# Kernel tuning notes

Measured on AMD Instinct MI355X. Metric: run time of the kernel, lower is better.

Reference implementation:

```python
import jax, jax.numpy as jnp
import numpy as np

B, T, D_IN = 64, 4096, 3
C1, H, NCLS = 64, 128, 40
BN_EPS = 1e-5


def setup_inputs() -> dict:
    key = jax.random.key(0)
    ks = jax.random.split(key, 12)
    s_ih = 1.0 / np.sqrt(C1)
    s_hh = 1.0 / np.sqrt(H)
    return {
        "x": jax.random.normal(ks[0], (B, T, D_IN), jnp.float32),
        "conv_w": jax.random.normal(ks[1], (C1, D_IN), jnp.float32) * 0.3,
        "conv_b": jax.random.normal(ks[2], (C1,), jnp.float32) * 0.1,
        "bn_gamma": jnp.ones((C1,), jnp.float32),
        "bn_beta": jnp.zeros((C1,), jnp.float32),
        "w_ih": jax.random.normal(ks[3], (4 * H, C1), jnp.float32) * s_ih,
        "b_ih": jax.random.normal(ks[4], (4 * H,), jnp.float32) * s_ih,
        "w_hh": jax.random.normal(ks[5], (4 * H, H), jnp.float32) * s_hh,
        "b_hh": jax.random.normal(ks[6], (4 * H,), jnp.float32) * s_hh,
        "out_w": jax.random.normal(ks[7], (NCLS, H), jnp.float32) * s_hh,
        "out_b": jax.random.normal(ks[8], (NCLS,), jnp.float32) * s_hh,
        "h0": jax.random.normal(ks[9], (B, H), jnp.float32),
        "c0": jax.random.normal(ks[10], (B, H), jnp.float32),
    }


def reference(x, conv_w, conv_b, bn_gamma, bn_beta, w_ih, b_ih, w_hh, b_hh,
              out_w, out_b, h0, c0):
    # Conv1d with kernel_size=1 == pointwise linear over channel dim.
    y = jnp.einsum('btc,oc->bto', x, conv_w) + conv_b  # [B, T, 64]
    # BatchNorm1d in training mode: batch stats over (batch, length).
    mean = jnp.mean(y, axis=(0, 1))
    var = jnp.var(y, axis=(0, 1))  # biased, matches torch BN normalization
    y = (y - mean) * jax.lax.rsqrt(var + BN_EPS) * bn_gamma + bn_beta
    y = jax.nn.relu(y)

    def step(carry, xt):
        h, c = carry
        gates = xt @ w_ih.T + b_ih + h @ w_hh.T + b_hh  # [B, 4H]
        i, f, g, o = jnp.split(gates, 4, axis=-1)
        c = jax.nn.sigmoid(f) * c + jax.nn.sigmoid(i) * jnp.tanh(g)
        h = jax.nn.sigmoid(o) * jnp.tanh(c)
        return (h, c), None

    (hT, _), _ = jax.lax.scan(step, (h0, c0), jnp.swapaxes(y, 0, 1))
    # Only the last hidden state feeds the classifier (output[:, -1, :]).
    return hT @ out_w.T + out_b  # [B, 40]
```

## Files before the change

kernel.cpp:

```cpp
#include <hip/hip_runtime.h>
#include <cstdint>
#include <cstddef>

#define B_    64
#define T_    4096
#define H_    128
#define C1_   64
#define NCLS_ 40

#define LOG2E_     1.4426950408889634f
#define TWOLOG2E_  2.8853900817779268f
#define NEG4LOG2E_ (-5.7707801635558536f)

typedef _Float16 half2_t __attribute__((ext_vector_type(2)));
typedef _Float16 half8_t __attribute__((ext_vector_type(8)));
typedef float    f32x4_t __attribute__((ext_vector_type(4)));

__device__ __forceinline__ half2_t pack2(float a, float b){
  half2_t r; r.x = (_Float16)a; r.y = (_Float16)b; return r;
}

__global__ __launch_bounds__(256) void stats_kernel(const float* __restrict__ x,
                                                    float* __restrict__ stats){
  int t = blockIdx.x * 256 + threadIdx.x;
  const float4* xv = (const float4*)x + (size_t)t * 3;
  float4 a = xv[0], b = xv[1], c = xv[2];
  float x0[4] = {a.x, a.w, b.z, c.y};
  float x1[4] = {a.y, b.x, b.w, c.z};
  float x2[4] = {a.z, b.y, c.x, c.w};
  float s[9] = {0,0,0,0,0,0,0,0,0};
  #pragma unroll
  for (int r=0;r<4;++r){
    s[0]+=x0[r]; s[1]+=x1[r]; s[2]+=x2[r];
    s[3]+=x0[r]*x0[r]; s[4]+=x0[r]*x1[r]; s[5]+=x0[r]*x2[r];
    s[6]+=x1[r]*x1[r]; s[7]+=x1[r]*x2[r]; s[8]+=x2[r]*x2[r];
  }
  __shared__ float red[9][256];
  #pragma unroll
  for (int j=0;j<9;++j) red[j][threadIdx.x] = s[j];
  __syncthreads();
  if (threadIdx.x < 9){
    float sum = 0.f;
    for (int i=0;i<256;++i) sum += red[threadIdx.x][i];
    atomicAdd(&stats[threadIdx.x], sum);
  }
}

__device__ __forceinline__ void chan_affine(int c, const float* __restrict__ conv_w,
    const float* __restrict__ bn_g, const float* __restrict__ bn_b,
    const float* __restrict__ stats,
    float& A0, float& A1, float& A2, float& Bc){
  const float Ninv = 1.0f / (float)(B_*T_);
  float m0=stats[0]*Ninv, m1=stats[1]*Ninv, m2=stats[2]*Ninv;
  float c00=stats[3]*Ninv-m0*m0, c01=stats[4]*Ninv-m0*m1, c02=stats[5]*Ninv-m0*m2;
  float c11=stats[6]*Ninv-m1*m1, c12=stats[7]*Ninv-m1*m2, c22=stats[8]*Ninv-m2*m2;
  float w0=conv_w[c*3+0], w1=conv_w[c*3+1], w2=conv_w[c*3+2];
  float var = w0*(w0*c00 + 2.f*(w1*c01 + w2*c02)) + w1*(w1*c11 + 2.f*w2*c12) + w2*w2*c22;
  float sc = bn_g[c] * rsqrtf(var + 1e-5f);
  A0 = w0*sc; A1 = w1*sc; A2 = w2*sc;
  Bc = bn_b[c] - (w0*m0 + w1*m1 + w2*m2)*sc;
}

__global__ __launch_bounds__(512,2) void lstm_fused_kernel(
    const float* __restrict__ x,
    const float* __restrict__ conv_w, const float* __restrict__ bn_g,
    const float* __restrict__ bn_b, const float* __restrict__ stats,
    const float* __restrict__ w_ih, const float* __restrict__ b_ih,
    const float* __restrict__ b_hh, const float* __restrict__ w_hh,
    const float* __restrict__ h0, const float* __restrict__ c0,
    const float* __restrict__ out_w, const float* __restrict__ out_b,
    float* __restrict__ out){
  constexpr int CH   = 16;
  constexpr int PSTR = 516;
  int b = blockIdx.x, t = threadIdx.x;
  int lane = t & 63, wv = t >> 6;
  int rfrag = lane & 15, kgrp = lane >> 4;
  int estar = wv*16 + rfrag;
  bool wrt = (kgrp == 0);

  __shared__ __align__(16) _Float16 hbuf[2][H_];
  __shared__ __align__(16) float P_lds[CH * PSTR];
  __shared__ __align__(16) float4 cf_lds[C1_];

  if (t < C1_){
    float A0,A1,A2,Bc; chan_affine(t, conv_w, bn_g, bn_b, stats, A0,A1,A2,Bc);
    cf_lds[t] = make_float4(A0,A1,A2,Bc);
  }

  half8_t Wf[4][4];
  #pragma unroll
  for (int g=0; g<4; ++g){
    float sg = (g==2) ? TWOLOG2E_ : -LOG2E_;
    #pragma unroll
    for (int kc=0; kc<4; ++kc){
      const float4* wp = (const float4*)(w_hh + (size_t)(g*H_ + wv*16 + rfrag)*H_ + kc*32 + kgrp*8);
      float4 u0 = wp[0], u1 = wp[1];
      half8_t hv;
      hv[0]=(_Float16)(sg*u0.x); hv[1]=(_Float16)(sg*u0.y);
      hv[2]=(_Float16)(sg*u0.z); hv[3]=(_Float16)(sg*u0.w);
      hv[4]=(_Float16)(sg*u1.x); hv[5]=(_Float16)(sg*u1.y);
      hv[6]=(_Float16)(sg*u1.z); hv[7]=(_Float16)(sg*u1.w);
      Wf[g][kc] = hv;
    }
  }
  half8_t bf[4][2];
  float sgb[4];
  #pragma unroll
  for (int g=0; g<4; ++g){
    int n = g*H_ + wv*16 + rfrag;
    float sg = (g==2) ? TWOLOG2E_ : -LOG2E_;
    sgb[g] = sg * (b_ih[n] + b_hh[n]);
    #pragma unroll
    for (int kh=0; kh<2; ++kh){
      const float4* wp = (const float4*)(w_ih + (size_t)n*C1_ + kh*32 + kgrp*8);
      float4 u0 = wp[0], u1 = wp[1];
      half8_t hv;
      hv[0]=(_Float16)(sg*u0.x); hv[1]=(_Float16)(sg*u0.y);
      hv[2]=(_Float16)(sg*u0.z); hv[3]=(_Float16)(sg*u0.w);
      hv[4]=(_Float16)(sg*u1.x); hv[5]=(_Float16)(sg*u1.y);
      hv[6]=(_Float16)(sg*u1.z); hv[7]=(_Float16)(sg*u1.w);
      bf[g][kh] = hv;
    }
  }

  float cs = TWOLOG2E_ * c0[(size_t)b*H_ + estar];
  if (wrt) hbuf[0][estar] = (_Float16)h0[(size_t)b*H_ + estar];

  const float* xb = x + (size_t)b*T_*3;
  float xp0, xp1, xp2;
  { const float* p = xb + 3*rfrag; xp0 = p[0]; xp1 = p[1]; xp2 = p[2]; }
  const f32x4_t Z = {0.f, 0.f, 0.f, 0.f};
  __syncthreads();

  for (int c = 0; c < T_/CH; ++c){
    half8_t a0, a1;
    #pragma unroll
    for (int j=0;j<8;++j){
      float4 q = cf_lds[kgrp*8+j];
      a0[j] = (_Float16)fmaxf(fmaf(q.x,xp0, fmaf(q.y,xp1, fmaf(q.z,xp2, q.w))), 0.f);
      float4 rr = cf_lds[32+kgrp*8+j];
      a1[j] = (_Float16)fmaxf(fmaf(rr.x,xp0, fmaf(rr.y,xp1, fmaf(rr.z,xp2, rr.w))), 0.f);
    }
    { int row = (c+1)*CH + rfrag; row = (row < T_) ? row : (T_-1);
      const float* p = xb + 3*row; xp0 = p[0]; xp1 = p[1]; xp2 = p[2]; }
    #pragma unroll
    for (int g=0; g<4; ++g){
      f32x4_t dp = __builtin_amdgcn_mfma_f32_16x16x32_f16(a0, bf[g][0], Z, 0, 0, 0);
      dp = __builtin_amdgcn_mfma_f32_16x16x32_f16(a1, bf[g][1], dp, 0, 0, 0);
      int col = (wv*16 + rfrag)*4 + g;
      #pragma unroll
      for (int v4=0; v4<4; ++v4)
        P_lds[(kgrp*4 + v4)*PSTR + col] = dp[v4] + sgb[g];
    }
    asm volatile("s_waitcnt lgkmcnt(0)" ::: "memory");
    __builtin_amdgcn_s_barrier();
    asm volatile("" ::: "memory");

    f32x4_t pq = *(const f32x4_t*)(P_lds + (size_t)estar*4);

    #pragma unroll
    for (int s=0; s<CH; ++s){
      int p = s & 1;
      if (s > 0){
        asm volatile("s_waitcnt lgkmcnt(0)" ::: "memory");
        __builtin_amdgcn_s_barrier();
        asm volatile("" ::: "memory");
      }
      const _Float16* hb = hbuf[p];
      uint4 hu0 = *(const uint4*)(hb + 0*32 + kgrp*8);
      uint4 hu1 = *(const uint4*)(hb + 1*32 + kgrp*8);
      uint4 hu2 = *(const uint4*)(hb + 2*32 + kgrp*8);
      uint4 hu3 = *(const uint4*)(hb + 3*32 + kgrp*8);
      f32x4_t pqn = pq;
      if (s < CH-1) pqn = *(const f32x4_t*)(P_lds + (size_t)(s+1)*PSTR + estar*4);
      half8_t A0 = __builtin_bit_cast(half8_t, hu0);
      half8_t A1 = __builtin_bit_cast(half8_t, hu1);
      half8_t A2 = __builtin_bit_cast(half8_t, hu2);
      half8_t A3 = __builtin_bit_cast(half8_t, hu3);
      f32x4_t d0 = __builtin_amdgcn_mfma_f32_16x16x32_f16(A0, Wf[0][0], Z, 0,0,0);
      f32x4_t d1 = __builtin_amdgcn_mfma_f32_16x16x32_f16(A0, Wf[1][0], Z, 0,0,0);
      f32x4_t d2 = __builtin_amdgcn_mfma_f32_16x16x32_f16(A0, Wf[2][0], Z, 0,0,0);
      f32x4_t d3 = __builtin_amdgcn_mfma_f32_16x16x32_f16(A0, Wf[3][0], Z, 0,0,0);
      d0 = __builtin_amdgcn_mfma_f32_16x16x32_f16(A1, Wf[0][1], d0, 0,0,0);
      d1 = __builtin_amdgcn_mfma_f32_16x16x32_f16(A1, Wf[1][1], d1, 0,0,0);
      d2 = __builtin_amdgcn_mfma_f32_16x16x32_f16(A1, Wf[2][1], d2, 0,0,0);
      d3 = __builtin_amdgcn_mfma_f32_16x16x32_f16(A1, Wf[3][1], d3, 0,0,0);
      d0 = __builtin_amdgcn_mfma_f32_16x16x32_f16(A2, Wf[0][2], d0, 0,0,0);
      d1 = __builtin_amdgcn_mfma_f32_16x16x32_f16(A2, Wf[1][2], d1, 0,0,0);
      d2 = __builtin_amdgcn_mfma_f32_16x16x32_f16(A2, Wf[2][2], d2, 0,0,0);
      d3 = __builtin_amdgcn_mfma_f32_16x16x32_f16(A2, Wf[3][2], d3, 0,0,0);
      d0 = __builtin_amdgcn_mfma_f32_16x16x32_f16(A3, Wf[0][3], d0, 0,0,0);
      d1 = __builtin_amdgcn_mfma_f32_16x16x32_f16(A3, Wf[1][3], d1, 0,0,0);
      d2 = __builtin_amdgcn_mfma_f32_16x16x32_f16(A3, Wf[2][3], d2, 0,0,0);
      d3 = __builtin_amdgcn_mfma_f32_16x16x32_f16(A3, Wf[3][3], d3, 0,0,0);
      float vI = d0[0] + pq[0];
      float vF = d1[0] + pq[1];
      float vG = d2[0] + pq[2];
      float vO = d3[0] + pq[3];
      float rI = __builtin_amdgcn_rcpf(1.f + __builtin_amdgcn_exp2f(vI));
      float rF = __builtin_amdgcn_rcpf(1.f + __builtin_amdgcn_exp2f(vF));
      float rG = __builtin_amdgcn_rcpf(1.f + __builtin_amdgcn_exp2f(vG));
      float rO = __builtin_amdgcn_rcpf(1.f + __builtin_amdgcn_exp2f(vO));
      float gT2 = fmaf(NEG4LOG2E_, rG, TWOLOG2E_);
      float cn  = fmaf(rF, cs, rI * gT2);
      cs = cn;
      float th = fmaf(-2.f, __builtin_amdgcn_rcpf(1.f + __builtin_amdgcn_exp2f(cn)), 1.f);
      float h  = rO * th;
      if (wrt) hbuf[1-p][estar] = (_Float16)h;
      pq = pqn;
    }
  }
  __syncthreads();
  if (t < NCLS_){
    float s = out_b[t];
    #pragma unroll 8
    for (int kk=0; kk<H_; ++kk)
      s = fmaf(out_w[t*H_ + kk], (float)hbuf[0][kk], s);
    out[(size_t)b*NCLS_ + t] = s;
  }
}

extern "C" void kernel_launch(void* const* d_in, const int* in_sizes, int n_in,
                              void* d_out, int out_size, void* d_ws, size_t ws_size,
                              hipStream_t stream){
  const float* x      = (const float*)d_in[0];
  const float* conv_w = (const float*)d_in[1];
  const float* bn_g   = (const float*)d_in[3];
  const float* bn_b   = (const float*)d_in[4];
  const float* w_ih   = (const float*)d_in[5];
  const float* b_ih   = (const float*)d_in[6];
  const float* w_hh   = (const float*)d_in[7];
  const float* b_hh   = (const float*)d_in[8];
  const float* out_w  = (const float*)d_in[9];
  const float* out_b  = (const float*)d_in[10];
  const float* h0     = (const float*)d_in[11];
  const float* c0     = (const float*)d_in[12];
  float* out   = (float*)d_out;
  float* stats = (float*)d_ws;

  hipMemsetAsync(d_ws, 0, 64, stream);
  stats_kernel<<<256, 256, 0, stream>>>(x, stats);
  lstm_fused_kernel<<<B_, 512, 0, stream>>>(x, conv_w, bn_g, bn_b, stats,
                                            w_ih, b_ih, b_hh, w_hh, h0, c0,
                                            out_w, out_b, out);
}
```

Baseline: 1.684 ms.

## Halve LSTM block to 4 waves, each computing 32 hidden units per step

The fused LSTM kernel now runs 256 threads (4 waves) per batch element instead of 512. Each wave holds recurrent and input weight fragments for two 16-unit tiles and issues 32 MFMAs per timestep. Lanes pick their tile's result with a select, and the P_lds precompute stores become float4 vector writes. The aim is a cheaper per-step barrier across fewer waves, at the cost of doubled MFMA work per wave, roughly double the weight registers, and idle lanes in the gate math.

Measured after the change: 1.856 ms. 1.1x slower.

```diff
diff --git a/kernel.cpp b/kernel.cpp
--- a/kernel.cpp
+++ b/kernel.cpp
@@ -61,7 +61,7 @@
   Bc = bn_b[c] - (w0*m0 + w1*m1 + w2*m2)*sc;
 }
 
-__global__ __launch_bounds__(512,2) void lstm_fused_kernel(
+__global__ __launch_bounds__(256,1) void lstm_fused_kernel(
     const float* __restrict__ x,
     const float* __restrict__ conv_w, const float* __restrict__ bn_g,
     const float* __restrict__ bn_b, const float* __restrict__ stats,
@@ -75,8 +75,10 @@
   int b = blockIdx.x, t = threadIdx.x;
   int lane = t & 63, wv = t >> 6;
   int rfrag = lane & 15, kgrp = lane >> 4;
-  int estar = wv*16 + rfrag;
-  bool wrt = (kgrp == 0);
+  int etl = kgrp >> 1;
+  int estar = wv*32 + etl*16 + rfrag;
+  bool wrt = (kgrp & 1) == 0;
+  bool esel = (etl != 0);
 
   __shared__ __align__(16) _Float16 hbuf[2][H_];
   __shared__ __align__(16) float P_lds[CH * PSTR];
@@ -87,39 +89,45 @@
     cf_lds[t] = make_float4(A0,A1,A2,Bc);
   }
 
-  half8_t Wf[4][4];
+  half8_t Wf[4][2][4];
   #pragma unroll
   for (int g=0; g<4; ++g){
     float sg = (g==2) ? TWOLOG2E_ : -LOG2E_;
     #pragma unroll
-    for (int kc=0; kc<4; ++kc){
-      const float4* wp = (const float4*)(w_hh + (size_t)(g*H_ + wv*16 + rfrag)*H_ + kc*32 + kgrp*8);
-      float4 u0 = wp[0], u1 = wp[1];
-      half8_t hv;
-      hv[0]=(_Float16)(sg*u0.x); hv[1]=(_Float16)(sg*u0.y);
-      hv[2]=(_Float16)(sg*u0.z); hv[3]=(_Float16)(sg*u0.w);
-      hv[4]=(_Float16)(sg*u1.x); hv[5]=(_Float16)(sg*u1.y);
-      hv[6]=(_Float16)(sg*u1.z); hv[7]=(_Float16)(sg*u1.w);
-      Wf[g][kc] = hv;
-    }
-  }
-  half8_t bf[4][2];
-  float sgb[4];
+    for (int et=0; et<2; ++et){
+      #pragma unroll
+      for (int kc=0; kc<4; ++kc){
+        const float4* wp = (const float4*)(w_hh + (size_t)(g*H_ + wv*32 + et*16 + rfrag)*H_ + kc*32 + kgrp*8);
+        float4 u0 = wp[0], u1 = wp[1];
+        half8_t hv;
+        hv[0]=(_Float16)(sg*u0.x); hv[1]=(_Float16)(sg*u0.y);
+        hv[2]=(_Float16)(sg*u0.z); hv[3]=(_Float16)(sg*u0.w);
+        hv[4]=(_Float16)(sg*u1.x); hv[5]=(_Float16)(sg*u1.y);
+        hv[6]=(_Float16)(sg*u1.z); hv[7]=(_Float16)(sg*u1.w);
+        Wf[g][et][kc] = hv;
+      }
+    }
+  }
+  half8_t bf[4][2][2];
+  float sgb[4][2];
   #pragma unroll
   for (int g=0; g<4; ++g){
-    int n = g*H_ + wv*16 + rfrag;
     float sg = (g==2) ? TWOLOG2E_ : -LOG2E_;
-    sgb[g] = sg * (b_ih[n] + b_hh[n]);
-    #pragma unroll
-    for (int kh=0; kh<2; ++kh){
-      const float4* wp = (const float4*)(w_ih + (size_t)n*C1_ + kh*32 + kgrp*8);
-      float4 u0 = wp[0], u1 = wp[1];
-      half8_t hv;
-      hv[0]=(_Float16)(sg*u0.x); hv[1]=(_Float16)(sg*u0.y);
-      hv[2]=(_Float16)(sg*u0.z); hv[3]=(_Float16)(sg*u0.w);
-      hv[4]=(_Float16)(sg*u1.x); hv[5]=(_Float16)(sg*u1.y);
-      hv[6]=(_Float16)(sg*u1.z); hv[7]=(_Float16)(sg*u1.w);
-      bf[g][kh] = hv;
+    #pragma unroll
+    for (int et=0; et<2; ++et){
+      int n = g*H_ + wv*32 + et*16 + rfrag;
+      sgb[g][et] = sg * (b_ih[n] + b_hh[n]);
+      #pragma unroll
+      for (int kh=0; kh<2; ++kh){
+        const float4* wp = (const float4*)(w_ih + (size_t)n*C1_ + kh*32 + kgrp*8);
+        float4 u0 = wp[0], u1 = wp[1];
+        half8_t hv;
+        hv[0]=(_Float16)(sg*u0.x); hv[1]=(_Float16)(sg*u0.y);
+        hv[2]=(_Float16)(sg*u0.z); hv[3]=(_Float16)(sg*u0.w);
+        hv[4]=(_Float16)(sg*u1.x); hv[5]=(_Float16)(sg*u1.y);
+        hv[6]=(_Float16)(sg*u1.z); hv[7]=(_Float16)(sg*u1.w);
+        bf[g][et][kh] = hv;
+      }
     }
   }
 
@@ -143,14 +151,27 @@
     }
     { int row = (c+1)*CH + rfrag; row = (row < T_) ? row : (T_-1);
       const float* p = xb + 3*row; xp0 = p[0]; xp1 = p[1]; xp2 = p[2]; }
+    f32x4_t dp[4][2];
     #pragma unroll
     for (int g=0; g<4; ++g){
-      f32x4_t dp = __builtin_amdgcn_mfma_f32_16x16x32_f16(a0, bf[g][0], Z, 0, 0, 0);
-      dp = __builtin_amdgcn_mfma_f32_16x16x32_f16(a1, bf[g][1], dp, 0, 0, 0);
-      int col = (wv*16 + rfrag)*4 + g;
-      #pragma unroll
-      for (int v4=0; v4<4; ++v4)
-        P_lds[(kgrp*4 + v4)*PSTR + col] = dp[v4] + sgb[g];
+      #pragma unroll
+      for (int et=0; et<2; ++et){
+        f32x4_t d = __builtin_amdgcn_mfma_f32_16x16x32_f16(a0, bf[g][et][0], Z, 0, 0, 0);
+        dp[g][et]  = __builtin_amdgcn_mfma_f32_16x16x32_f16(a1, bf[g][et][1], d, 0, 0, 0);
+      }
+    }
+    #pragma unroll
+    for (int et=0; et<2; ++et){
+      int colbase = (wv*32 + et*16 + rfrag)*4;
+      #pragma unroll
+      for (int v4=0; v4<4; ++v4){
+        f32x4_t vec;
+        vec[0] = dp[0][et][v4] + sgb[0][et];
+        vec[1] = dp[1][et][v4] + sgb[1][et];
+        vec[2] = dp[2][et][v4] + sgb[2][et];
+        vec[3] = dp[3][et][v4] + sgb[3][et];
+        *(f32x4_t*)(P_lds + (size_t)(kgrp*4 + v4)*PSTR + colbase) = vec;
+      }
     }
     asm volatile("s_waitcnt lgkmcnt(0)" ::: "memory");
     __builtin_amdgcn_s_barrier();
@@ -177,26 +198,39 @@
       half8_t A1 = __builtin_bit_cast(half8_t, hu1);
       half8_t A2 = __builtin_bit_cast(half8_t, hu2);
       half8_t A3 = __builtin_bit_cast(half8_t, hu3);
-      f32x4_t d0 = __builtin_amdgcn_mfma_f32_16x16x32_f16(A0, Wf[0][0], Z, 0,0,0);
-      f32x4_t d1 = __builtin_amdgcn_mfma_f32_16x16x32_f16(A0, Wf[1][0], Z, 0,0,0);
-      f32x4_t d2 = __builtin_amdgcn_mfma_f32_16x16x32_f16(A0, Wf[2][0], Z, 0,0,0);
-      f32x4_t d3 = __builtin_amdgcn_mfma_f32_16x16x32_f16(A0, Wf[3][0], Z, 0,0,0);
-      d0 = __builtin_amdgcn_mfma_f32_16x16x32_f16(A1, Wf[0][1], d0, 0,0,0);
-      d1 = __builtin_amdgcn_mfma_f32_16x16x32_f16(A1, Wf[1][1], d1, 0,0,0);
-      d2 = __builtin_amdgcn_mfma_f32_16x16x32_f16(A1, Wf[2][1], d2, 0,0,0);
-      d3 = __builtin_amdgcn_mfma_f32_16x16x32_f16(A1, Wf[3][1], d3, 0,0,0);
-      d0 = __builtin_amdgcn_mfma_f32_16x16x32_f16(A2, Wf[0][2], d0, 0,0,0);
-      d1 = __builtin_amdgcn_mfma_f32_16x16x32_f16(A2, Wf[1][2], d1, 0,0,0);
-      d2 = __builtin_amdgcn_mfma_f32_16x16x32_f16(A2, Wf[2][2], d2, 0,0,0);
-      d3 = __builtin_amdgcn_mfma_f32_16x16x32_f16(A2, Wf[3][2], d3, 0,0,0);
-      d0 = __builtin_amdgcn_mfma_f32_16x16x32_f16(A3, Wf[0][3], d0, 0,0,0);
-      d1 = __builtin_amdgcn_mfma_f32_16x16x32_f16(A3, Wf[1][3], d1, 0,0,0);
-      d2 = __builtin_amdgcn_mfma_f32_16x16x32_f16(A3, Wf[2][3], d2, 0,0,0);
-      d3 = __builtin_amdgcn_mfma_f32_16x16x32_f16(A3, Wf[3][3], d3, 0,0,0);
-      float vI = d0[0] + pq[0];
-      float vF = d1[0] + pq[1];
-      float vG = d2[0] + pq[2];
-      float vO = d3[0] + pq[3];
+      f32x4_t d[4][2];
+      #pragma unroll
+      for (int g=0; g<4; ++g){
+        #pragma unroll
+        for (int et=0; et<2; ++et)
+          d[g][et] = __builtin_amdgcn_mfma_f32_16x16x32_f16(A0, Wf[g][et][0], Z, 0,0,0);
+      }
+      #pragma unroll
+      for (int g=0; g<4; ++g){
+        #pragma unroll
+        for (int et=0; et<2; ++et)
+          d[g][et] = __builtin_amdgcn_mfma_f32_16x16x32_f16(A1, Wf[g][et][1], d[g][et], 0,0,0);
+      }
+      #pragma unroll
+      for (int g=0; g<4; ++g){
+        #pragma unroll
+        for (int et=0; et<2; ++et)
+          d[g][et] = __builtin_amdgcn_mfma_f32_16x16x32_f16(A2, Wf[g][et][2], d[g][et], 0,0,0);
+      }
+      #pragma unroll
+      for (int g=0; g<4; ++g){
+        #pragma unroll
+        for (int et=0; et<2; ++et)
+          d[g][et] = __builtin_amdgcn_mfma_f32_16x16x32_f16(A3, Wf[g][et][3], d[g][et], 0,0,0);
+      }
+      float sI = esel ? d[0][1][0] : d[0][0][0];
+      float sF = esel ? d[1][1][0] : d[1][0][0];
+      float sG = esel ? d[2][1][0] : d[2][0][0];
+      float sO = esel ? d[3][1][0] : d[3][0][0];
+      float vI = sI + pq[0];
+      float vF = sF + pq[1];
+      float vG = sG + pq[2];
+      float vO = sO + pq[3];
       float rI = __builtin_amdgcn_rcpf(1.f + __builtin_amdgcn_exp2f(vI));
       float rF = __builtin_amdgcn_rcpf(1.f + __builtin_amdgcn_exp2f(vF));
       float rG = __builtin_amdgcn_rcpf(1.f + __builtin_amdgcn_exp2f(vG));
@@ -240,7 +274,7 @@
 
   hipMemsetAsync(d_ws, 0, 64, stream);
   stats_kernel<<<256, 256, 0, stream>>>(x, stats);
-  lstm_fused_kernel<<<B_, 512, 0, stream>>>(x, conv_w, bn_g, bn_b, stats,
+  lstm_fused_kernel<<<B_, 256, 0, stream>>>(x, conv_w, bn_g, bn_b, stats,
                                             w_ih, b_ih, b_hh, w_hh, h0, c0,
                                             out_w, out_b, out);
 }
```

## Load hidden state once and broadcast via DPP; split MFMA accumulation chains

Applied to the files above, without the earlier changes.

Each lane now issues a single 16-byte LDS read of the hidden-state slice and uses quad DPP broadcasts to assemble the four A operands, instead of four separate LDS reads per step. The four-deep dependent MFMA accumulation chains are split into two independent chains of two, summed afterwards. Both aim to shorten the per-timestep critical path of the serial recurrence, at the cost of extra DPP VALU instructions and more accumulator registers.

Measured after the change: 2.241 ms. 33.1% more time.

```diff
diff --git a/kernel.cpp b/kernel.cpp
--- a/kernel.cpp
+++ b/kernel.cpp
@@ -18,6 +18,10 @@
 
 __device__ __forceinline__ half2_t pack2(float a, float b){
   half2_t r; r.x = (_Float16)a; r.y = (_Float16)b; return r;
+}
+template<int CTRL>
+__device__ __forceinline__ unsigned qdpp(unsigned x){
+  return (unsigned)__builtin_amdgcn_update_dpp(0, (int)x, CTRL, 0xF, 0xF, true);
 }
 
 __global__ __launch_bounds__(256) void stats_kernel(const float* __restrict__ x,
@@ -130,6 +134,7 @@
   float xp0, xp1, xp2;
   { const float* p = xb + 3*rfrag; xp0 = p[0]; xp1 = p[1]; xp2 = p[2]; }
   const f32x4_t Z = {0.f, 0.f, 0.f, 0.f};
+  int hsl = (lane & 3)*32 + kgrp*8;
   __syncthreads();
 
   for (int c = 0; c < T_/CH; ++c){
@@ -166,37 +171,38 @@
         __builtin_amdgcn_s_barrier();
         asm volatile("" ::: "memory");
       }
-      const _Float16* hb = hbuf[p];
-      uint4 hu0 = *(const uint4*)(hb + 0*32 + kgrp*8);
-      uint4 hu1 = *(const uint4*)(hb + 1*32 + kgrp*8);
-      uint4 hu2 = *(const uint4*)(hb + 2*32 + kgrp*8);
-      uint4 hu3 = *(const uint4*)(hb + 3*32 + kgrp*8);
+      uint4 hr = *(const uint4*)(hbuf[p] + hsl);
       f32x4_t pqn = pq;
       if (s < CH-1) pqn = *(const f32x4_t*)(P_lds + (size_t)(s+1)*PSTR + estar*4);
-      half8_t A0 = __builtin_bit_cast(half8_t, hu0);
-      half8_t A1 = __builtin_bit_cast(half8_t, hu1);
-      half8_t A2 = __builtin_bit_cast(half8_t, hu2);
-      half8_t A3 = __builtin_bit_cast(half8_t, hu3);
-      f32x4_t d0 = __builtin_amdgcn_mfma_f32_16x16x32_f16(A0, Wf[0][0], Z, 0,0,0);
-      f32x4_t d1 = __builtin_amdgcn_mfma_f32_16x16x32_f16(A0, Wf[1][0], Z, 0,0,0);
-      f32x4_t d2 = __builtin_amdgcn_mfma_f32_16x16x32_f16(A0, Wf[2][0], Z, 0,0,0);
-      f32x4_t d3 = __builtin_amdgcn_mfma_f32_16x16x32_f16(A0, Wf[3][0], Z, 0,0,0);
-      d0 = __builtin_amdgcn_mfma_f32_16x16x32_f16(A1, Wf[0][1], d0, 0,0,0);
-      d1 = __builtin_amdgcn_mfma_f32_16x16x32_f16(A1, Wf[1][1], d1, 0,0,0);
-      d2 = __builtin_amdgcn_mfma_f32_16x16x32_f16(A1, Wf[2][1], d2, 0,0,0);
-      d3 = __builtin_amdgcn_mfma_f32_16x16x32_f16(A1, Wf[3][1], d3, 0,0,0);
-      d0 = __builtin_amdgcn_mfma_f32_16x16x32_f16(A2, Wf[0][2], d0, 0,0,0);
-      d1 = __builtin_amdgcn_mfma_f32_16x16x32_f16(A2, Wf[1][2], d1, 0,0,0);
-      d2 = __builtin_amdgcn_mfma_f32_16x16x32_f16(A2, Wf[2][2], d2, 0,0,0);
-      d3 = __builtin_amdgcn_mfma_f32_16x16x32_f16(A2, Wf[3][2], d3, 0,0,0);
-      d0 = __builtin_amdgcn_mfma_f32_16x16x32_f16(A3, Wf[0][3], d0, 0,0,0);
-      d1 = __builtin_amdgcn_mfma_f32_16x16x32_f16(A3, Wf[1][3], d1, 0,0,0);
-      d2 = __builtin_amdgcn_mfma_f32_16x16x32_f16(A3, Wf[2][3], d2, 0,0,0);
-      d3 = __builtin_amdgcn_mfma_f32_16x16x32_f16(A3, Wf[3][3], d3, 0,0,0);
-      float vI = d0[0] + pq[0];
-      float vF = d1[0] + pq[1];
-      float vG = d2[0] + pq[2];
-      float vO = d3[0] + pq[3];
+      uint4 u0, u1, u2, u3;
+      u0.x = qdpp<0x00>(hr.x); u0.y = qdpp<0x00>(hr.y); u0.z = qdpp<0x00>(hr.z); u0.w = qdpp<0x00>(hr.w);
+      u1.x = qdpp<0x55>(hr.x); u1.y = qdpp<0x55>(hr.y); u1.z = qdpp<0x55>(hr.z); u1.w = qdpp<0x55>(hr.w);
+      u2.x = qdpp<0xAA>(hr.x); u2.y = qdpp<0xAA>(hr.y); u2.z = qdpp<0xAA>(hr.z); u2.w = qdpp<0xAA>(hr.w);
+      u3.x = qdpp<0xFF>(hr.x); u3.y = qdpp<0xFF>(hr.y); u3.z = qdpp<0xFF>(hr.z); u3.w = qdpp<0xFF>(hr.w);
+      half8_t A0 = __builtin_bit_cast(half8_t, u0);
+      half8_t A1 = __builtin_bit_cast(half8_t, u1);
+      half8_t A2 = __builtin_bit_cast(half8_t, u2);
+      half8_t A3 = __builtin_bit_cast(half8_t, u3);
+      f32x4_t dA0 = __builtin_amdgcn_mfma_f32_16x16x32_f16(A0, Wf[0][0], Z, 0,0,0);
+      f32x4_t dA1 = __builtin_amdgcn_mfma_f32_16x16x32_f16(A0, Wf[1][0], Z, 0,0,0);
+      f32x4_t dA2 = __builtin_amdgcn_mfma_f32_16x16x32_f16(A0, Wf[2][0], Z, 0,0,0);
+      f32x4_t dA3 = __builtin_amdgcn_mfma_f32_16x16x32_f16(A0, Wf[3][0], Z, 0,0,0);
+      f32x4_t dB0 = __builtin_amdgcn_mfma_f32_16x16x32_f16(A1, Wf[0][1], Z, 0,0,0);
+      f32x4_t dB1 = __builtin_amdgcn_mfma_f32_16x16x32_f16(A1, Wf[1][1], Z, 0,0,0);
+      f32x4_t dB2 = __builtin_amdgcn_mfma_f32_16x16x32_f16(A1, Wf[2][1], Z, 0,0,0);
+      f32x4_t dB3 = __builtin_amdgcn_mfma_f32_16x16x32_f16(A1, Wf[3][1], Z, 0,0,0);
+      dA0 = __builtin_amdgcn_mfma_f32_16x16x32_f16(A2, Wf[0][2], dA0, 0,0,0);
+      dA1 = __builtin_amdgcn_mfma_f32_16x16x32_f16(A2, Wf[1][2], dA1, 0,0,0);
+      dA2 = __builtin_amdgcn_mfma_f32_16x16x32_f16(A2, Wf[2][2], dA2, 0,0,0);
+      dA3 = __builtin_amdgcn_mfma_f32_16x16x32_f16(A2, Wf[3][2], dA3, 0,0,0);
+      dB0 = __builtin_amdgcn_mfma_f32_16x16x32_f16(A3, Wf[0][3], dB0, 0,0,0);
+      dB1 = __builtin_amdgcn_mfma_f32_16x16x32_f16(A3, Wf[1][3], dB1, 0,0,0);
+      dB2 = __builtin_amdgcn_mfma_f32_16x16x32_f16(A3, Wf[2][3], dB2, 0,0,0);
+      dB3 = __builtin_amdgcn_mfma_f32_16x16x32_f16(A3, Wf[3][3], dB3, 0,0,0);
+      float vI = (dA0[0] + dB0[0]) + pq[0];
+      float vF = (dA1[0] + dB1[0]) + pq[1];
+      float vG = (dA2[0] + dB2[0]) + pq[2];
+      float vO = (dA3[0] + dB3[0]) + pq[3];
       float rI = __builtin_amdgcn_rcpf(1.f + __builtin_amdgcn_exp2f(vI));
       float rF = __builtin_amdgcn_rcpf(1.f + __builtin_amdgcn_exp2f(vF));
       float rG = __builtin_amdgcn_rcpf(1.f + __builtin_amdgcn_exp2f(vG));
```

## Process two batch sequences per block to interleave independent LSTM recurrences

Applied to the files above, without the earlier changes.

Each block now handles two batch elements, doubling shared-memory h and preactivation buffers and running both recurrences within the same per-step barrier. The intent is to hide MFMA and transcendental latency of one sequence's serial chain behind the other's and to amortize barrier cost per sequence. It halves the grid and raises register and LDS pressure, and the per-step critical path lengthens if the compiler does not interleave the two chains.

Measured after the change: 3.657 ms. 117% more time.

```diff
diff --git a/kernel.cpp b/kernel.cpp
--- a/kernel.cpp
+++ b/kernel.cpp
@@ -72,14 +72,14 @@
     float* __restrict__ out){
   constexpr int CH   = 16;
   constexpr int PSTR = 516;
-  int b = blockIdx.x, t = threadIdx.x;
+  int bb = blockIdx.x * 2, t = threadIdx.x;
   int lane = t & 63, wv = t >> 6;
   int rfrag = lane & 15, kgrp = lane >> 4;
   int estar = wv*16 + rfrag;
   bool wrt = (kgrp == 0);
 
-  __shared__ __align__(16) _Float16 hbuf[2][H_];
-  __shared__ __align__(16) float P_lds[CH * PSTR];
+  __shared__ __align__(16) _Float16 hbuf[2][2][H_];
+  __shared__ __align__(16) float P_lds[2][CH * PSTR];
   __shared__ __align__(16) float4 cf_lds[C1_];
 
   if (t < C1_){
@@ -123,40 +123,49 @@
     }
   }
 
-  float cs = TWOLOG2E_ * c0[(size_t)b*H_ + estar];
-  if (wrt) hbuf[0][estar] = (_Float16)h0[(size_t)b*H_ + estar];
-
-  const float* xb = x + (size_t)b*T_*3;
-  float xp0, xp1, xp2;
-  { const float* p = xb + 3*rfrag; xp0 = p[0]; xp1 = p[1]; xp2 = p[2]; }
+  float cs[2];
+  float xp[2][3];
+  #pragma unroll
+  for (int ch=0; ch<2; ++ch){
+    cs[ch] = TWOLOG2E_ * c0[(size_t)(bb+ch)*H_ + estar];
+    if (wrt) hbuf[ch][0][estar] = (_Float16)h0[(size_t)(bb+ch)*H_ + estar];
+    const float* p = x + ((size_t)(bb+ch)*T_ + rfrag)*3;
+    xp[ch][0] = p[0]; xp[ch][1] = p[1]; xp[ch][2] = p[2];
+  }
   const f32x4_t Z = {0.f, 0.f, 0.f, 0.f};
   __syncthreads();
 
   for (int c = 0; c < T_/CH; ++c){
-    half8_t a0, a1;
-    #pragma unroll
-    for (int j=0;j<8;++j){
-      float4 q = cf_lds[kgrp*8+j];
-      a0[j] = (_Float16)fmaxf(fmaf(q.x,xp0, fmaf(q.y,xp1, fmaf(q.z,xp2, q.w))), 0.f);
-      float4 rr = cf_lds[32+kgrp*8+j];
-      a1[j] = (_Float16)fmaxf(fmaf(rr.x,xp0, fmaf(rr.y,xp1, fmaf(rr.z,xp2, rr.w))), 0.f);
-    }
-    { int row = (c+1)*CH + rfrag; row = (row < T_) ? row : (T_-1);
-      const float* p = xb + 3*row; xp0 = p[0]; xp1 = p[1]; xp2 = p[2]; }
-    #pragma unroll
-    for (int g=0; g<4; ++g){
-      f32x4_t dp = __builtin_amdgcn_mfma_f32_16x16x32_f16(a0, bf[g][0], Z, 0, 0, 0);
-      dp = __builtin_amdgcn_mfma_f32_16x16x32_f16(a1, bf[g][1], dp, 0, 0, 0);
-      int col = (wv*16 + rfrag)*4 + g;
-      #pragma unroll
-      for (int v4=0; v4<4; ++v4)
-        P_lds[(kgrp*4 + v4)*PSTR + col] = dp[v4] + sgb[g];
+    #pragma unroll
+    for (int ch=0; ch<2; ++ch){
+      half8_t a0, a1;
+      #pragma unroll
+      for (int j=0;j<8;++j){
+        float4 q = cf_lds[kgrp*8+j];
+        a0[j] = (_Float16)fmaxf(fmaf(q.x,xp[ch][0], fmaf(q.y,xp[ch][1], fmaf(q.z,xp[ch][2], q.w))), 0.f);
+        float4 rr = cf_lds[32+kgrp*8+j];
+        a1[j] = (_Float16)fmaxf(fmaf(rr.x,xp[ch][0], fmaf(rr.y,xp[ch][1], fmaf(rr.z,xp[ch][2], rr.w))), 0.f);
+      }
+      { int row = (c+1)*CH + rfrag; row = (row < T_) ? row : (T_-1);
+        const float* p = x + ((size_t)(bb+ch)*T_ + row)*3;
+        xp[ch][0] = p[0]; xp[ch][1] = p[1]; xp[ch][2] = p[2]; }
+      #pragma unroll
+      for (int g=0; g<4; ++g){
+        f32x4_t dp = __builtin_amdgcn_mfma_f32_16x16x32_f16(a0, bf[g][0], Z, 0, 0, 0);
+        dp = __builtin_amdgcn_mfma_f32_16x16x32_f16(a1, bf[g][1], dp, 0, 0, 0);
+        int col = (wv*16 + rfrag)*4 + g;
+        #pragma unroll
+        for (int v4=0; v4<4; ++v4)
+          P_lds[ch][(kgrp*4 + v4)*PSTR + col] = dp[v4] + sgb[g];
+      }
     }
     asm volatile("s_waitcnt lgkmcnt(0)" ::: "memory");
     __builtin_amdgcn_s_barrier();
     asm volatile("" ::: "memory");
 
-    f32x4_t pq = *(const f32x4_t*)(P_lds + (size_t)estar*4);
+    f32x4_t pq[2];
+    pq[0] = *(const f32x4_t*)(P_lds[0] + (size_t)estar*4);
+    pq[1] = *(const f32x4_t*)(P_lds[1] + (size_t)estar*4);
 
     #pragma unroll
     for (int s=0; s<CH; ++s){
@@ -166,57 +175,70 @@
         __builtin_amdgcn_s_barrier();
         asm volatile("" ::: "memory");
       }
-      const _Float16* hb = hbuf[p];
-      uint4 hu0 = *(const uint4*)(hb + 0*32 + kgrp*8);
-      uint4 hu1 = *(const uint4*)(hb + 1*32 + kgrp*8);
-      uint4 hu2 = *(const uint4*)(hb + 2*32 + kgrp*8);
-      uint4 hu3 = *(const uint4*)(hb + 3*32 + kgrp*8);
-      f32x4_t pqn = pq;
-      if (s < CH-1) pqn = *(const f32x4_t*)(P_lds + (size_t)(s+1)*PSTR + estar*4);
-      half8_t A0 = __builtin_bit_cast(half8_t, hu0);
-      half8_t A1 = __builtin_bit_cast(half8_t, hu1);
-      half8_t A2 = __builtin_bit_cast(half8_t, hu2);
-      half8_t A3 = __builtin_bit_cast(half8_t, hu3);
-      f32x4_t d0 = __builtin_amdgcn_mfma_f32_16x16x32_f16(A0, Wf[0][0], Z, 0,0,0);
-      f32x4_t d1 = __builtin_amdgcn_mfma_f32_16x16x32_f16(A0, Wf[1][0], Z, 0,0,0);
-      f32x4_t d2 = __builtin_amdgcn_mfma_f32_16x16x32_f16(A0, Wf[2][0], Z, 0,0,0);
-      f32x4_t d3 = __builtin_amdgcn_mfma_f32_16x16x32_f16(A0, Wf[3][0], Z, 0,0,0);
-      d0 = __builtin_amdgcn_mfma_f32_16x16x32_f16(A1, Wf[0][1], d0, 0,0,0);
-      d1 = __builtin_amdgcn_mfma_f32_16x16x32_f16(A1, Wf[1][1], d1, 0,0,0);
-      d2 = __builtin_amdgcn_mfma_f32_16x16x32_f16(A1, Wf[2][1], d2, 0,0,0);
-      d3 = __builtin_amdgcn_mfma_f32_16x16x32_f16(A1, Wf[3][1], d3, 0,0,0);
-      d0 = __builtin_amdgcn_mfma_f32_16x16x32_f16(A2, Wf[0][2], d0, 0,0,0);
-      d1 = __builtin_amdgcn_mfma_f32_16x16x32_f16(A2, Wf[1][2], d1, 0,0,0);
-      d2 = __builtin_amdgcn_mfma_f32_16x16x32_f16(A2, Wf[2][2], d2, 0,0,0);
-      d3 = __builtin_amdgcn_mfma_f32_16x16x32_f16(A2, Wf[3][2], d3, 0,0,0);
-      d0 = __builtin_amdgcn_mfma_f32_16x16x32_f16(A3, Wf[0][3], d0, 0,0,0);
-      d1 = __builtin_amdgcn_mfma_f32_16x16x32_f16(A3, Wf[1][3], d1, 0,0,0);
-      d2 = __builtin_amdgcn_mfma_f32_16x16x32_f16(A3, Wf[2][3], d2, 0,0,0);
-      d3 = __builtin_amdgcn_mfma_f32_16x16x32_f16(A3, Wf[3][3], d3, 0,0,0);
-      float vI = d0[0] + pq[0];
-      float vF = d1[0] + pq[1];
-      float vG = d2[0] + pq[2];
-      float vO = d3[0] + pq[3];
-      float rI = __builtin_amdgcn_rcpf(1.f + __builtin_amdgcn_exp2f(vI));
-      float rF = __builtin_amdgcn_rcpf(1.f + __builtin_amdgcn_exp2f(vF));
-      float rG = __builtin_amdgcn_rcpf(1.f + __builtin_amdgcn_exp2f(vG));
-      float rO = __builtin_amdgcn_rcpf(1.f + __builtin_amdgcn_exp2f(vO));
-      float gT2 = fmaf(NEG4LOG2E_, rG, TWOLOG2E_);
-      float cn  = fmaf(rF, cs, rI * gT2);
-      cs = cn;
-      float th = fmaf(-2.f, __builtin_amdgcn_rcpf(1.f + __builtin_amdgcn_exp2f(cn)), 1.f);
-      float h  = rO * th;
-      if (wrt) hbuf[1-p][estar] = (_Float16)h;
-      pq = pqn;
+      uint4 hu[2][4];
+      #pragma unroll
+      for (int ch=0; ch<2; ++ch){
+        const _Float16* hb = hbuf[ch][p];
+        hu[ch][0] = *(const uint4*)(hb + 0*32 + kgrp*8);
+        hu[ch][1] = *(const uint4*)(hb + 1*32 + kgrp*8);
+        hu[ch][2] = *(const uint4*)(hb + 2*32 + kgrp*8);
+        hu[ch][3] = *(const uint4*)(hb + 3*32 + kgrp*8);
+      }
+      f32x4_t pqn[2] = {pq[0], pq[1]};
+      if (s < CH-1){
+        pqn[0] = *(const f32x4_t*)(P_lds[0] + (size_t)(s+1)*PSTR + estar*4);
+        pqn[1] = *(const f32x4_t*)(P_lds[1] + (size_t)(s+1)*PSTR + estar*4);
+      }
+      #pragma unroll
+      for (int ch=0; ch<2; ++ch){
+        half8_t A0 = __builtin_bit_cast(half8_t, hu[ch][0]);
+        half8_t A1 = __builtin_bit_cast(half8_t, hu[ch][1]);
+        half8_t A2 = __builtin_bit_cast(half8_t, hu[ch][2]);
+        half8_t A3 = __builtin_bit_cast(half8_t, hu[ch][3]);
+        f32x4_t d0 = __builtin_amdgcn_mfma_f32_16x16x32_f16(A0, Wf[0][0], Z, 0,0,0);
+        f32x4_t d1 = __builtin_amdgcn_mfma_f32_16x16x32_f16(A0, Wf[1][0], Z, 0,0,0);
+        f32x4_t d2 = __builtin_amdgcn_mfma_f32_16x16x32_f16(A0, Wf[2][0], Z, 0,0,0);
+        f32x4_t d3 = __builtin_amdgcn_mfma_f32_16x16x32_f16(A0, Wf[3][0], Z, 0,0,0);
+        d0 = __builtin_amdgcn_mfma_f32_16x16x32_f16(A1, Wf[0][1], d0, 0,0,0);
+        d1 = __builtin_amdgcn_mfma_f32_16x16x32_f16(A1, Wf[1][1], d1, 0,0,0);
+        d2 = __builtin_amdgcn_mfma_f32_16x16x32_f16(A1, Wf[2][1], d2, 0,0,0);
+        d3 = __builtin_amdgcn_mfma_f32_16x16x32_f16(A1, Wf[3][1], d3, 0,0,0);
+        d0 = __builtin_amdgcn_mfma_f32_16x16x32_f16(A2, Wf[0][2], d0, 0,0,0);
+        d1 = __builtin_amdgcn_mfma_f32_16x16x32_f16(A2, Wf[1][2], d1, 0,0,0);
+        d2 = __builtin_amdgcn_mfma_f32_16x16x32_f16(A2, Wf[2][2], d2, 0,0,0);
+        d3 = __builtin_amdgcn_mfma_f32_16x16x32_f16(A2, Wf[3][2], d3, 0,0,0);
+        d0 = __builtin_amdgcn_mfma_f32_16x16x32_f16(A3, Wf[0][3], d0, 0,0,0);
+        d1 = __builtin_amdgcn_mfma_f32_16x16x32_f16(A3, Wf[1][3], d1, 0,0,0);
+        d2 = __builtin_amdgcn_mfma_f32_16x16x32_f16(A3, Wf[2][3], d2, 0,0,0);
+        d3 = __builtin_amdgcn_mfma_f32_16x16x32_f16(A3, Wf[3][3], d3, 0,0,0);
+        float vI = d0[0] + pq[ch][0];
+        float vF = d1[0] + pq[ch][1];
+        float vG = d2[0] + pq[ch][2];
+        float vO = d3[0] + pq[ch][3];
+        float rI = __builtin_amdgcn_rcpf(1.f + __builtin_amdgcn_exp2f(vI));
+        float rF = __builtin_amdgcn_rcpf(1.f + __builtin_amdgcn_exp2f(vF));
+        float rG = __builtin_amdgcn_rcpf(1.f + __builtin_amdgcn_exp2f(vG));
+        float rO = __builtin_amdgcn_rcpf(1.f + __builtin_amdgcn_exp2f(vO));
+        float gT2 = fmaf(NEG4LOG2E_, rG, TWOLOG2E_);
+        float cn  = fmaf(rF, cs[ch], rI * gT2);
+        cs[ch] = cn;
+        float th = fmaf(-2.f, __builtin_amdgcn_rcpf(1.f + __builtin_amdgcn_exp2f(cn)), 1.f);
+        float h  = rO * th;
+        if (wrt) hbuf[ch][1-p][estar] = (_Float16)h;
+        pq[ch] = pqn[ch];
+      }
     }
   }
   __syncthreads();
   if (t < NCLS_){
-    float s = out_b[t];
-    #pragma unroll 8
-    for (int kk=0; kk<H_; ++kk)
-      s = fmaf(out_w[t*H_ + kk], (float)hbuf[0][kk], s);
-    out[(size_t)b*NCLS_ + t] = s;
+    #pragma unroll
+    for (int ch=0; ch<2; ++ch){
+      float s = out_b[t];
+      #pragma unroll 8
+      for (int kk=0; kk<H_; ++kk)
+        s = fmaf(out_w[t*H_ + kk], (float)hbuf[ch][0][kk], s);
+      out[(size_t)(bb+ch)*NCLS_ + t] = s;
+    }
   }
 }
 
@@ -240,7 +262,7 @@
 
   hipMemsetAsync(d_ws, 0, 64, stream);
   stats_kernel<<<256, 256, 0, stream>>>(x, stats);
-  lstm_fused_kernel<<<B_, 512, 0, stream>>>(x, conv_w, bn_g, bn_b, stats,
-                                            w_ih, b_ih, b_hh, w_hh, h0, c0,
-                                            out_w, out_b, out);
-}
+  lstm_fused_kernel<<<B_/2, 512, 0, stream>>>(x, conv_w, bn_g, bn_b, stats,
+                                              w_ih, b_ih, b_hh, w_hh, h0, c0,
+                                              out_w, out_b, out);
+}
```
